# Kernel optimization log

Hardware: AMD Instinct MI355X
Metric: run time of the kernel (lower is better)

Reference implementation:

```python
import jax, jax.numpy as jnp
import numpy as np

SIZE = 161          # odd box size (init arg 160 -> 161)
INPUT_SIZE = 8
BATCH = 256
MARGIN = 3          # VOXEL_SPREAD_MARGIN


def _radial_expansion(grid):
    # verbatim numpy port of SparseVolumeReconstructionLinear.radial_expansion
    bz = grid.shape[0]
    bz2 = bz // 2
    mask1 = grid == -1
    ls = np.linspace(-bz2, bz2, bz)
    lsx = np.linspace(0, bz2, bz // 2 + 1)
    z, y, x = np.meshgrid(ls, ls, lsx)
    c = np.zeros((int(np.sum(mask1)), 3))
    c[:, 0] = x[mask1]
    c[:, 1] = y[mask1]
    c[:, 2] = z[mask1]
    norm = np.sqrt(np.sum(np.square(c), axis=1))
    c_ = np.round(c / norm[:, None]).astype(int)
    c = c.astype(int)
    c[:, 1:] += bz2
    c_ = c - c_
    g = grid[c_[:, 2], c_[:, 1], c_[:, 0]]
    mask2 = g >= 0
    grid[c[mask2, 2], c[mask2, 1], c[mask2, 0]] = g[mask2]


def _build_grid3d_index(size):
    bz = size
    bz_2 = bz // 2
    zz = (np.arange(bz) - bz_2) ** 2
    yy = (np.arange(bz) - bz_2) ** 2
    xx = np.arange(bz_2 + 1) ** 2
    mask = (zz[:, None, None] + yy[None, :, None] + xx[None, None, :]) <= bz_2 ** 2
    # C-order enumeration matches grid_iterator(z, y, x) ordering
    idx = np.cumsum(mask.ravel()).reshape(mask.shape) - 1
    grid = np.where(mask, idx, -1).astype(np.int64)
    m = MARGIN
    bzm = bz + 2 * m
    gm = np.full((bzm, bzm, bzm // 2 + 1), -1, dtype=np.int64)
    gm[m:-m, m:-m, :-m] = grid
    for _ in range(5):
        _radial_expansion(gm)
    return gm, int(mask.sum())


def _rand_rotations(key, n):
    q = jax.random.normal(key, (n, 4))
    q = q / jnp.linalg.norm(q, axis=1, keepdims=True)
    w, x, y, z = q[:, 0], q[:, 1], q[:, 2], q[:, 3]
    R = jnp.stack([
        1 - 2 * (y * y + z * z), 2 * (x * y - z * w), 2 * (x * z + y * w),
        2 * (x * y + z * w), 1 - 2 * (x * x + z * z), 2 * (y * z - x * w),
        2 * (x * z - y * w), 2 * (y * z + x * w), 1 - 2 * (x * x + y * y),
    ], axis=-1).reshape(n, 3, 3)
    return R.astype(jnp.float32)


def setup_inputs() -> dict:
    key = jax.random.key(0)
    k1, k2, k3, k4 = jax.random.split(key, 4)
    grid3d_index, weight_count = _build_grid3d_index(SIZE)
    weight = jax.random.normal(k1, (weight_count, INPUT_SIZE, 2), dtype=jnp.float32) * 1e-3
    bias = jax.random.normal(k2, (weight_count, 2), dtype=jnp.float32) * 1e-3
    inp = jax.random.normal(k3, (BATCH, INPUT_SIZE), dtype=jnp.float32)
    rot = _rand_rotations(k4, BATCH)
    # half-plane 2D Fourier coords (x >= 0), P = SIZE * (SIZE//2 + 1)
    ys, xs = np.meshgrid(np.arange(SIZE) - SIZE // 2, np.arange(SIZE // 2 + 1), indexing='ij')
    coord = np.stack([xs.ravel(), ys.ravel()], axis=-1).astype(np.float32)
    return {
        'input': inp,
        'weight': weight,
        'bias': bias,
        'grid3d_index': jnp.asarray(grid3d_index),
        'rot_matrices': rot,
        'grid2d_coord': jnp.asarray(coord),
        'max_r': SIZE // 2,
    }


def reference(input, weight, bias, grid3d_index, rot_matrices, grid2d_coord, max_r):
    # input: (B, D); weight: (W, D, 2); bias: (W, 2)
    # grid2d_coord: (P, 2) as (x, y); rot_matrices: (B, 3, 3)
    bz = grid3d_index.shape[0]
    bz2 = bz // 2
    mr = min(int(max_r), (bz - 2 * MARGIN) // 2)
    P = grid2d_coord.shape[0]
    # rotate the z=0 plane into 3D Fourier space: (B, P, 3) as (x, y, z)
    c2 = jnp.pad(grid2d_coord, ((0, 0), (0, 1)))
    c = jnp.einsum('bij,pj->bpi', rot_matrices, c2)
    # Hermitian symmetry: flip to x >= 0 half-grid, conjugate
    flip = c[..., 0] < 0
    c = jnp.where(flip[..., None], -c, c)
    valid = jnp.sum(grid2d_coord ** 2, axis=-1) <= float(mr * mr)  # (P,)
    c = jnp.where(valid[None, :, None], c, 0.0)
    f = jnp.floor(c)
    t = c - f                      # trilinear fractions (B, P, 3)
    fi = f.astype(jnp.int32)
    out = jnp.zeros((c.shape[0], P, 2), dtype=input.dtype)
    for dx in (0, 1):
        wx = t[..., 0] if dx else 1.0 - t[..., 0]
        for dy in (0, 1):
            wy = t[..., 1] if dy else 1.0 - t[..., 1]
            for dz in (0, 1):
                wz = t[..., 2] if dz else 1.0 - t[..., 2]
                xi = fi[..., 0] + dx
                yi = fi[..., 1] + dy + bz2
                zi = fi[..., 2] + dz + bz2
                j = grid3d_index[zi, yi, xi]        # (B, P) voxel ids, -1 = empty
                jm = jnp.maximum(j, 0)
                v = jnp.einsum('bd,bpdc->bpc', input, weight[jm]) + bias[jm]
                v = jnp.where((j >= 0)[..., None], v, 0.0)
                out = out + (wx * wy * wz)[..., None] * v
    imag_sign = jnp.where(flip, -1.0, 1.0)
    out = out * jnp.stack([jnp.ones_like(imag_sign), imag_sign], axis=-1)
    return jnp.where(valid[None, :, None], out, 0.0)
```

## Files before the change

kernel.cpp:

```cpp
#include <hip/hip_runtime.h>

#define BZ    167
#define BZ2   83
#define NX    84
#define NCELL (BZ * BZ * NX)
#define SYC   NX
#define SZC   (NX * BZ)
#define NXC   81
#define NYC   161
#define NTX   21
#define NTY   41
#define NTILE (NTX * NTY)
#define NBT   216
#define NBX   51

static __device__ __forceinline__ unsigned f2bf(float f) {
    unsigned u = __float_as_uint(f);
    return (u + 0x7FFFu + ((u >> 16) & 1u)) >> 16;
}
static __device__ __forceinline__ float bf_lo(unsigned u) {
    return __uint_as_float(u << 16);
}
static __device__ __forceinline__ float bf_hi(unsigned u) {
    return __uint_as_float(u & 0xFFFF0000u);
}

__global__ __launch_bounds__(256) void pack_allz(
    const float4* __restrict__ wsrc, uint2* __restrict__ wdst, int nw4, int nbw,
    const int* __restrict__ grid, const float* __restrict__ bias,
    int4* __restrict__ garrD, int ncell)
{
    if ((int)blockIdx.x < nbw) {
        const int i = blockIdx.x * 256 + threadIdx.x;
        if (i >= nw4) return;
        const float4 v = wsrc[i];
        wdst[i] = make_uint2(f2bf(v.x) | (f2bf(v.y) << 16),
                             f2bf(v.z) | (f2bf(v.w) << 16));
    } else {
        const int i = ((int)blockIdx.x - nbw) * 256 + threadIdx.x;
        if (i >= ncell) return;
        const int j0 = grid[i];
        const int j1 = (i + SZC < ncell) ? grid[i + SZC] : -1;
        unsigned b0 = 0u, b1 = 0u;
        if (j0 >= 0)
            b0 = f2bf(bias[2 * j0]) | (f2bf(bias[2 * j0 + 1]) << 16);
        if (j1 >= 0)
            b1 = f2bf(bias[2 * j1]) | (f2bf(bias[2 * j1 + 1]) << 16);
        garrD[i] = make_int4(j0, (int)b0, j1, (int)b1);
    }
}

__global__ __launch_bounds__(256, 4) void svr_tile(
    const float*    __restrict__ input,
    const unsigned* __restrict__ wpk,
    const int4*     __restrict__ garrD,
    const float*    __restrict__ rot,
    const float*    __restrict__ coord,
    const int*      __restrict__ max_r,
    float*          __restrict__ out,
    int P)
{
    const int m    = blockIdx.x;
    const int xcd  = m & 7;
    const int slot = m >> 3;
    const int b    = (slot / NBT) * 8 + xcd;
    const int tgrp = slot % NBT;
    const int wid  = threadIdx.x >> 6;
    const int lane = threadIdx.x & 63;
    const int t    = tgrp * 4 + wid;
    if (t >= NTILE) return;

    const int q    = lane & 3;
    const int h    = q & 1;
    const int dxl  = q >> 1;
    const int sub  = lane >> 2;
    const int px   = (t % NTX) * 4 + (sub & 3);
    const int py   = (t / NTX) * 4 + (sub >> 2);
    if (px >= NXC || py >= NYC) return;
    const int p    = py * NXC + px;

    const float2 xy = *(const float2*)(coord + 2 * p);
    const float x = xy.x, y = xy.y;

    const int mr = min(max_r[0], (BZ - 6) / 2);
    const bool valid = (x * x + y * y) <= (float)(mr * mr);

    float2* o = (float2*)(out + ((size_t)b * P + p) * 2);
    if (!valid) {
        if (q == 0) *o = make_float2(0.f, 0.f);
        return;
    }

    const float* R = rot + b * 9;
    float cx = fmaf(R[1], y, R[0] * x);
    float cy = fmaf(R[4], y, R[3] * x);
    float cz = fmaf(R[7], y, R[6] * x);

    float sgn = 1.f;
    if (cx < 0.f) { cx = -cx; cy = -cy; cz = -cz; sgn = -1.f; }

    const float fx = floorf(cx), fy = floorf(cy), fz = floorf(cz);
    const float tx = cx - fx, ty = cy - fy, tz = cz - fz;
    const int ix = (int)fx;
    const int iy = (int)fy + BZ2;
    const int iz = (int)fz + BZ2;

    const int base0 = (iz * BZ + iy) * NX + ix + dxl;
    const int4 Gd0 = garrD[base0];
    const int4 Gd1 = garrD[base0 + SYC];

    const float4 ih = *(const float4*)(input + b * 8 + h * 4);

    const float wxd = dxl ? tx : 1.f - tx;
    float wyz[4];
    wyz[0] = (1.f - ty) * (1.f - tz);
    wyz[1] = ty * (1.f - tz);
    wyz[2] = (1.f - ty) * tz;
    wyz[3] = ty * tz;

    int jraw[4]; unsigned bbl[4];
    jraw[0] = Gd0.x; bbl[0] = (unsigned)Gd0.y;
    jraw[1] = Gd1.x; bbl[1] = (unsigned)Gd1.y;
    jraw[2] = Gd0.z; bbl[2] = (unsigned)Gd0.w;
    jraw[3] = Gd1.z; bbl[3] = (unsigned)Gd1.w;

    int jj[4]; float wcl[4];
    #pragma unroll
    for (int i = 0; i < 4; ++i) {
        wcl[i] = (jraw[i] >= 0) ? wxd * wyz[i] : 0.f;
        jj[i]  = max(jraw[i], 0);
    }

    uint4 U[4];
    #pragma unroll
    for (int i = 0; i < 4; ++i)
        U[i] = *(const uint4*)(wpk + (size_t)jj[i] * 8 + h * 4);

    float acc0 = 0.f, acc1 = 0.f;
    #pragma unroll
    for (int i = 0; i < 4; ++i) {
        const float w = wcl[i];
        const unsigned bb = bbl[i];
        float v0 = h ? 0.f : bf_lo(bb);
        float v1 = h ? 0.f : bf_hi(bb);
        v0 = fmaf(ih.x, bf_lo(U[i].x), v0); v1 = fmaf(ih.x, bf_hi(U[i].x), v1);
        v0 = fmaf(ih.y, bf_lo(U[i].y), v0); v1 = fmaf(ih.y, bf_hi(U[i].y), v1);
        v0 = fmaf(ih.z, bf_lo(U[i].z), v0); v1 = fmaf(ih.z, bf_hi(U[i].z), v1);
        v0 = fmaf(ih.w, bf_lo(U[i].w), v0); v1 = fmaf(ih.w, bf_hi(U[i].w), v1);
        acc0 = fmaf(w, v0, acc0);
        acc1 = fmaf(w, v1, acc1);
    }

    acc0 += __shfl_xor(acc0, 1);
    acc1 += __shfl_xor(acc1, 1);
    acc0 += __shfl_xor(acc0, 2);
    acc1 += __shfl_xor(acc1, 2);

    if (q == 0) *o = make_float2(acc0, acc1 * sgn);
}

__global__ __launch_bounds__(256) void pack_w(
    const float4* __restrict__ src, uint2* __restrict__ dst, int n)
{
    const int i = blockIdx.x * 256 + threadIdx.x;
    if (i >= n) return;
    const float4 v = src[i];
    dst[i] = make_uint2(f2bf(v.x) | (f2bf(v.y) << 16),
                        f2bf(v.z) | (f2bf(v.w) << 16));
}
__global__ __launch_bounds__(256) void pack_b(
    const float* __restrict__ bias, unsigned* __restrict__ bpk, int W)
{
    const int j = blockIdx.x * 256 + threadIdx.x;
    if (j >= W) return;
    bpk[j] = f2bf(bias[2 * j]) | (f2bf(bias[2 * j + 1]) << 16);
}

__global__ __launch_bounds__(256) void svr_bf16(
    const float* __restrict__ input, const unsigned* __restrict__ wpk,
    const unsigned* __restrict__ bpk, const int* __restrict__ grid3d,
    const float* __restrict__ rot, const float* __restrict__ coord,
    const int* __restrict__ max_r, float* __restrict__ out, int P)
{
    const int m    = blockIdx.x;
    const int xcd  = m & 7;
    const int slot = m >> 3;
    const int b    = (slot / NBX) * 8 + xcd;
    const int p    = (slot % NBX) * 256 + threadIdx.x;
    if (p >= P) return;

    const float x = coord[2 * p + 0];
    const float y = coord[2 * p + 1];
    const int mr = min(max_r[0], (BZ - 6) / 2);
    const bool valid = (x * x + y * y) <= (float)(mr * mr);
    float2* o = (float2*)(out + ((size_t)b * P + p) * 2);
    if (!valid) { *o = make_float2(0.f, 0.f); return; }

    const float* R = rot + b * 9;
    float cx = fmaf(R[1], y, R[0] * x);
    float cy = fmaf(R[4], y, R[3] * x);
    float cz = fmaf(R[7], y, R[6] * x);
    float sgn = 1.f;
    if (cx < 0.f) { cx = -cx; cy = -cy; cz = -cz; sgn = -1.f; }
    const float fx = floorf(cx), fy = floorf(cy), fz = floorf(cz);
    const float tx = cx - fx, ty = cy - fy, tz = cz - fz;
    const int ix = (int)fx, iy = (int)fy + BZ2, iz = (int)fz + BZ2;

    const float* ib = input + b * 8;
    const float in0 = ib[0], in1 = ib[1], in2 = ib[2], in3 = ib[3];
    const float in4 = ib[4], in5 = ib[5], in6 = ib[6], in7 = ib[7];

    int jj[8]; float wc[8];
    const float wx0 = 1.f - tx, wy0 = 1.f - ty, wz0 = 1.f - tz;
    #pragma unroll
    for (int dz = 0; dz < 2; ++dz)
        #pragma unroll
        for (int dy = 0; dy < 2; ++dy) {
            const int base = ((iz + dz) * BZ + (iy + dy)) * NX + ix;
            #pragma unroll
            for (int dx = 0; dx < 2; ++dx) {
                const int c = dz * 4 + dy * 2 + dx;
                const int j = grid3d[base + dx];
                const float w = (dx ? tx : wx0) * (dy ? ty : wy0) * (dz ? tz : wz0);
                wc[c] = (j >= 0) ? w : 0.f;
                jj[c] = max(j, 0);
            }
        }

    uint4 U0[8], U1[8]; unsigned BB[8];
    #pragma unroll
    for (int c = 0; c < 8; ++c) {
        const uint4* wp = (const uint4*)(wpk + (size_t)jj[c] * 8);
        U0[c] = wp[0]; U1[c] = wp[1]; BB[c] = bpk[jj[c]];
    }

    float acc0 = 0.f, acc1 = 0.f;
    #pragma unroll
    for (int c = 0; c < 8; ++c) {
        const float w = wc[c];
        float v0 = bf_lo(BB[c]), v1 = bf_hi(BB[c]);
        v0 = fmaf(in0, bf_lo(U0[c].x), v0); v1 = fmaf(in0, bf_hi(U0[c].x), v1);
        v0 = fmaf(in1, bf_lo(U0[c].y), v0); v1 = fmaf(in1, bf_hi(U0[c].y), v1);
        v0 = fmaf(in2, bf_lo(U0[c].z), v0); v1 = fmaf(in2, bf_hi(U0[c].z), v1);
        v0 = fmaf(in3, bf_lo(U0[c].w), v0); v1 = fmaf(in3, bf_hi(U0[c].w), v1);
        v0 = fmaf(in4, bf_lo(U1[c].x), v0); v1 = fmaf(in4, bf_hi(U1[c].x), v1);
        v0 = fmaf(in5, bf_lo(U1[c].y), v0); v1 = fmaf(in5, bf_hi(U1[c].y), v1);
        v0 = fmaf(in6, bf_lo(U1[c].z), v0); v1 = fmaf(in6, bf_hi(U1[c].z), v1);
        v0 = fmaf(in7, bf_lo(U1[c].w), v0); v1 = fmaf(in7, bf_hi(U1[c].w), v1);
        acc0 = fmaf(w, v0, acc0);
        acc1 = fmaf(w, v1, acc1);
    }
    *o = make_float2(acc0, acc1 * sgn);
}

__global__ __launch_bounds__(256) void svr_fp32(
    const float* __restrict__ input, const float* __restrict__ weight,
    const float* __restrict__ bias, const int* __restrict__ grid3d,
    const float* __restrict__ rot, const float* __restrict__ coord,
    const int* __restrict__ max_r, float* __restrict__ out, int P)
{
    const int m    = blockIdx.x;
    const int xcd  = m & 7;
    const int slot = m >> 3;
    const int b    = (slot / NBX) * 8 + xcd;
    const int p    = (slot % NBX) * 256 + threadIdx.x;
    if (p >= P) return;

    const float x = coord[2 * p + 0];
    const float y = coord[2 * p + 1];
    const int mr = min(max_r[0], (BZ - 6) / 2);
    const bool valid = (x * x + y * y) <= (float)(mr * mr);
    float2* o = (float2*)(out + ((size_t)b * P + p) * 2);
    if (!valid) { *o = make_float2(0.f, 0.f); return; }

    const float* R = rot + b * 9;
    float cx = fmaf(R[1], y, R[0] * x);
    float cy = fmaf(R[4], y, R[3] * x);
    float cz = fmaf(R[7], y, R[6] * x);
    float sgn = 1.f;
    if (cx < 0.f) { cx = -cx; cy = -cy; cz = -cz; sgn = -1.f; }
    const float fx = floorf(cx), fy = floorf(cy), fz = floorf(cz);
    const float tx = cx - fx, ty = cy - fy, tz = cz - fz;
    const int ix = (int)fx, iy = (int)fy + BZ2, iz = (int)fz + BZ2;

    const float* ib = input + b * 8;
    const float in0 = ib[0], in1 = ib[1], in2 = ib[2], in3 = ib[3];
    const float in4 = ib[4], in5 = ib[5], in6 = ib[6], in7 = ib[7];

    int jj[8]; float wc[8];
    const float wx0 = 1.f - tx, wy0 = 1.f - ty, wz0 = 1.f - tz;
    #pragma unroll
    for (int dz = 0; dz < 2; ++dz)
        #pragma unroll
        for (int dy = 0; dy < 2; ++dy) {
            const int base = ((iz + dz) * BZ + (iy + dy)) * NX + ix;
            #pragma unroll
            for (int dx = 0; dx < 2; ++dx) {
                const int c = dz * 4 + dy * 2 + dx;
                const int j = grid3d[base + dx];
                const float w = (dx ? tx : wx0) * (dy ? ty : wy0) * (dz ? tz : wz0);
                wc[c] = (j >= 0) ? w : 0.f;
                jj[c] = max(j, 0);
            }
        }

    float acc0 = 0.f, acc1 = 0.f;
    #pragma unroll
    for (int c = 0; c < 8; ++c) {
        const size_t j = (size_t)jj[c];
        const float4* wp = (const float4*)(weight + j * 16);
        const float4 W0 = wp[0], W1 = wp[1], W2 = wp[2], W3 = wp[3];
        const float2 bb = *(const float2*)(bias + j * 2);
        const float w = wc[c];
        float v0 = bb.x, v1 = bb.y;
        v0 = fmaf(in0, W0.x, v0); v1 = fmaf(in0, W0.y, v1);
        v0 = fmaf(in1, W0.z, v0); v1 = fmaf(in1, W0.w, v1);
        v0 = fmaf(in2, W1.x, v0); v1 = fmaf(in2, W1.y, v1);
        v0 = fmaf(in3, W1.z, v0); v1 = fmaf(in3, W1.w, v1);
        v0 = fmaf(in4, W2.x, v0); v1 = fmaf(in4, W2.y, v1);
        v0 = fmaf(in5, W2.z, v0); v1 = fmaf(in5, W2.w, v1);
        v0 = fmaf(in6, W3.x, v0); v1 = fmaf(in6, W3.y, v1);
        v0 = fmaf(in7, W3.z, v0); v1 = fmaf(in7, W3.w, v1);
        acc0 = fmaf(w, v0, acc0);
        acc1 = fmaf(w, v1, acc1);
    }
    *o = make_float2(acc0, acc1 * sgn);
}

extern "C" void kernel_launch(void* const* d_in, const int* in_sizes, int n_in,
                              void* d_out, int out_size, void* d_ws, size_t ws_size,
                              hipStream_t stream) {
    const float* input  = (const float*)d_in[0];
    const float* weight = (const float*)d_in[1];
    const float* bias   = (const float*)d_in[2];
    const int*   grid3d = (const int*)  d_in[3];
    const float* rot    = (const float*)d_in[4];
    const float* coord  = (const float*)d_in[5];
    const int*   max_r  = (const int*)  d_in[6];
    float* out = (float*)d_out;

    const int P = in_sizes[5] / 2;
    const int B = in_sizes[4] / 9;
    const int W = in_sizes[1] / 16;

    const size_t wpk_bytes = (size_t)W * 32;
    const size_t need_zd   = wpk_bytes + (size_t)NCELL * 16;
    const size_t need_bf   = (size_t)W * 36;

    dim3 block(256, 1, 1);

    if (ws_size >= need_zd) {
        unsigned* wpk = (unsigned*)d_ws;
        int4* garrD = (int4*)((char*)d_ws + wpk_bytes);
        const int nw4 = W * 4;
        const int nbw = (nw4 + 255) / 256;
        const int nbg = (NCELL + 255) / 256;
        pack_allz<<<nbw + nbg, block, 0, stream>>>(
            (const float4*)weight, (uint2*)wpk, nw4, nbw,
            grid3d, bias, garrD, NCELL);
        dim3 grid(NBT * B, 1, 1);
        svr_tile<<<grid, block, 0, stream>>>(input, wpk, garrD, rot, coord,
                                             max_r, out, P);
    } else if (ws_size >= need_bf) {
        unsigned* wpk = (unsigned*)d_ws;
        unsigned* bpk = wpk + (size_t)W * 8;
        const int nw = W * 4;
        pack_w<<<(nw + 255) / 256, block, 0, stream>>>(
            (const float4*)weight, (uint2*)wpk, nw);
        pack_b<<<(W + 255) / 256, block, 0, stream>>>(bias, bpk, W);
        dim3 grid(NBX * B, 1, 1);
        svr_bf16<<<grid, block, 0, stream>>>(input, wpk, bpk, grid3d, rot,
                                             coord, max_r, out, P);
    } else {
        dim3 grid(NBX * B, 1, 1);
        svr_fp32<<<grid, block, 0, stream>>>(input, weight, bias, grid3d, rot,
                                             coord, max_r, out, P);
    }
}
```

Baseline: 220.7 us.

## Pack weights and input as fp16 and use packed dot2 instructions in gather kernel

Weights and the per-batch input vector are converted to packed fp16 pairs in the prep kernel, and the inner 4-term dot products use v_dot2 fp16 instructions instead of bf16 unpack plus scalar FMAs. The launch grid also changes from a 1D XCD-swizzled layout to a 3D grid of (batch, x-tile, y-tile group). This cuts ALU work in the per-corner dot product. It trades bf16 range for fp16 precision on weights and inputs, and drops the XCD-aware block mapping that may have aided L2 locality.

```diff
diff --git a/kernel.cpp b/kernel.cpp
--- a/kernel.cpp
+++ b/kernel.cpp
@@ -9,9 +9,7 @@
 #define NXC   81
 #define NYC   161
 #define NTX   21
-#define NTY   41
-#define NTILE (NTX * NTY)
-#define NBT   216
+#define NTZ   11
 #define NBX   51
 
 static __device__ __forceinline__ unsigned f2bf(float f) {
@@ -25,19 +23,30 @@
     return __uint_as_float(u & 0xFFFF0000u);
 }
 
-__global__ __launch_bounds__(256) void pack_allz(
+typedef _Float16 h2 __attribute__((ext_vector_type(2)));
+static __device__ __forceinline__ h2 u2h(unsigned u) {
+    union { unsigned u; h2 h; } x; x.u = u; return x.h;
+}
+static __device__ __forceinline__ unsigned f2h2(float a, float b) {
+    union { h2 h; unsigned u; } x;
+    x.h.x = (_Float16)a; x.h.y = (_Float16)b;
+    return x.u;
+}
+
+__global__ __launch_bounds__(256) void pack_allh(
     const float4* __restrict__ wsrc, uint2* __restrict__ wdst, int nw4, int nbw,
     const int* __restrict__ grid, const float* __restrict__ bias,
-    int4* __restrict__ garrD, int ncell)
-{
-    if ((int)blockIdx.x < nbw) {
-        const int i = blockIdx.x * 256 + threadIdx.x;
+    int4* __restrict__ garrD, int ncell, int nbg,
+    const float* __restrict__ input, unsigned* __restrict__ inpk, int nin)
+{
+    const int bid = (int)blockIdx.x;
+    if (bid < nbw) {
+        const int i = bid * 256 + threadIdx.x;
         if (i >= nw4) return;
         const float4 v = wsrc[i];
-        wdst[i] = make_uint2(f2bf(v.x) | (f2bf(v.y) << 16),
-                             f2bf(v.z) | (f2bf(v.w) << 16));
-    } else {
-        const int i = ((int)blockIdx.x - nbw) * 256 + threadIdx.x;
+        wdst[i] = make_uint2(f2h2(v.x, v.z), f2h2(v.y, v.w));
+    } else if (bid < nbw + nbg) {
+        const int i = (bid - nbw) * 256 + threadIdx.x;
         if (i >= ncell) return;
         const int j0 = grid[i];
         const int j1 = (i + SZC < ncell) ? grid[i + SZC] : -1;
@@ -47,11 +56,16 @@
         if (j1 >= 0)
             b1 = f2bf(bias[2 * j1]) | (f2bf(bias[2 * j1 + 1]) << 16);
         garrD[i] = make_int4(j0, (int)b0, j1, (int)b1);
-    }
-}
-
-__global__ __launch_bounds__(256, 4) void svr_tile(
-    const float*    __restrict__ input,
+    } else {
+        const int i = (bid - nbw - nbg) * 256 + threadIdx.x;
+        if (i >= nin) return;
+        const int b = i >> 2, k = i & 3;
+        inpk[i] = f2h2(input[b * 8 + 2 * k], input[b * 8 + 2 * k + 1]);
+    }
+}
+
+__global__ __launch_bounds__(256, 4) void svr_dot(
+    const unsigned* __restrict__ inpk,
     const unsigned* __restrict__ wpk,
     const int4*     __restrict__ garrD,
     const float*    __restrict__ rot,
@@ -60,22 +74,18 @@
     float*          __restrict__ out,
     int P)
 {
-    const int m    = blockIdx.x;
-    const int xcd  = m & 7;
-    const int slot = m >> 3;
-    const int b    = (slot / NBT) * 8 + xcd;
-    const int tgrp = slot % NBT;
+    const int b    = (int)blockIdx.x;
+    const int lane = threadIdx.x & 63;
     const int wid  = threadIdx.x >> 6;
-    const int lane = threadIdx.x & 63;
-    const int t    = tgrp * 4 + wid;
-    if (t >= NTILE) return;
+    const int ty   = (int)blockIdx.z * 4 + wid;
+    if (ty * 4 >= NYC) return;
 
     const int q    = lane & 3;
     const int h    = q & 1;
     const int dxl  = q >> 1;
     const int sub  = lane >> 2;
-    const int px   = (t % NTX) * 4 + (sub & 3);
-    const int py   = (t / NTX) * 4 + (sub >> 2);
+    const int px   = (int)blockIdx.y * 4 + (sub & 3);
+    const int py   = ty * 4 + (sub >> 2);
     if (px >= NXC || py >= NYC) return;
     const int p    = py * NXC + px;
 
@@ -100,7 +110,7 @@
     if (cx < 0.f) { cx = -cx; cy = -cy; cz = -cz; sgn = -1.f; }
 
     const float fx = floorf(cx), fy = floorf(cy), fz = floorf(cz);
-    const float tx = cx - fx, ty = cy - fy, tz = cz - fz;
+    const float tx = cx - fx, ty2 = cy - fy, tz = cz - fz;
     const int ix = (int)fx;
     const int iy = (int)fy + BZ2;
     const int iz = (int)fz + BZ2;
@@ -109,14 +119,16 @@
     const int4 Gd0 = garrD[base0];
     const int4 Gd1 = garrD[base0 + SYC];
 
-    const float4 ih = *(const float4*)(input + b * 8 + h * 4);
+    const uint2 ihu = *(const uint2*)(inpk + b * 4 + h * 2);
+    const h2 ihp0 = u2h(ihu.x);
+    const h2 ihp1 = u2h(ihu.y);
 
     const float wxd = dxl ? tx : 1.f - tx;
     float wyz[4];
-    wyz[0] = (1.f - ty) * (1.f - tz);
-    wyz[1] = ty * (1.f - tz);
-    wyz[2] = (1.f - ty) * tz;
-    wyz[3] = ty * tz;
+    wyz[0] = (1.f - ty2) * (1.f - tz);
+    wyz[1] = ty2 * (1.f - tz);
+    wyz[2] = (1.f - ty2) * tz;
+    wyz[3] = ty2 * tz;
 
     int jraw[4]; unsigned bbl[4];
     jraw[0] = Gd0.x; bbl[0] = (unsigned)Gd0.y;
@@ -139,16 +151,15 @@
     float acc0 = 0.f, acc1 = 0.f;
     #pragma unroll
     for (int i = 0; i < 4; ++i) {
-        const float w = wcl[i];
         const unsigned bb = bbl[i];
         float v0 = h ? 0.f : bf_lo(bb);
         float v1 = h ? 0.f : bf_hi(bb);
-        v0 = fmaf(ih.x, bf_lo(U[i].x), v0); v1 = fmaf(ih.x, bf_hi(U[i].x), v1);
-        v0 = fmaf(ih.y, bf_lo(U[i].y), v0); v1 = fmaf(ih.y, bf_hi(U[i].y), v1);
-        v0 = fmaf(ih.z, bf_lo(U[i].z), v0); v1 = fmaf(ih.z, bf_hi(U[i].z), v1);
-        v0 = fmaf(ih.w, bf_lo(U[i].w), v0); v1 = fmaf(ih.w, bf_hi(U[i].w), v1);
-        acc0 = fmaf(w, v0, acc0);
-        acc1 = fmaf(w, v1, acc1);
+        v0 = __builtin_amdgcn_fdot2(ihp0, u2h(U[i].x), v0, false);
+        v0 = __builtin_amdgcn_fdot2(ihp1, u2h(U[i].z), v0, false);
+        v1 = __builtin_amdgcn_fdot2(ihp0, u2h(U[i].y), v1, false);
+        v1 = __builtin_amdgcn_fdot2(ihp1, u2h(U[i].w), v1, false);
+        acc0 = fmaf(wcl[i], v0, acc0);
+        acc1 = fmaf(wcl[i], v1, acc1);
     }
 
     acc0 += __shfl_xor(acc0, 1);
@@ -343,24 +354,30 @@
     const int B = in_sizes[4] / 9;
     const int W = in_sizes[1] / 16;
 
-    const size_t wpk_bytes = (size_t)W * 32;
-    const size_t need_zd   = wpk_bytes + (size_t)NCELL * 16;
-    const size_t need_bf   = (size_t)W * 36;
+    const size_t wpk_bytes  = (size_t)W * 32;
+    const size_t garr_bytes = (size_t)NCELL * 16;
+    const size_t in_bytes   = (size_t)B * 16;
+    const size_t need_zd    = wpk_bytes + garr_bytes + in_bytes;
+    const size_t need_bf    = (size_t)W * 36;
 
     dim3 block(256, 1, 1);
 
-    if (ws_size >= need_zd) {
+    if (ws_size >= need_zd && P == NXC * NYC) {
         unsigned* wpk = (unsigned*)d_ws;
         int4* garrD = (int4*)((char*)d_ws + wpk_bytes);
+        unsigned* inpk = (unsigned*)((char*)d_ws + wpk_bytes + garr_bytes);
         const int nw4 = W * 4;
         const int nbw = (nw4 + 255) / 256;
         const int nbg = (NCELL + 255) / 256;
-        pack_allz<<<nbw + nbg, block, 0, stream>>>(
+        const int nin = B * 4;
+        const int nbi = (nin + 255) / 256;
+        pack_allh<<<nbw + nbg + nbi, block, 0, stream>>>(
             (const float4*)weight, (uint2*)wpk, nw4, nbw,
-            grid3d, bias, garrD, NCELL);
-        dim3 grid(NBT * B, 1, 1);
-        svr_tile<<<grid, block, 0, stream>>>(input, wpk, garrD, rot, coord,
-                                             max_r, out, P);
+            grid3d, bias, garrD, NCELL, nbg,
+            input, inpk, nin);
+        dim3 grid(B, NTX, NTZ);
+        svr_dot<<<grid, block, 0, stream>>>(inpk, wpk, garrD, rot, coord,
+                                            max_r, out, P);
     } else if (ws_size >= need_bf) {
         unsigned* wpk = (unsigned*)d_ws;
         unsigned* bpk = wpk + (size_t)W * 8;
```

Measured after the change: 224.8 us. Within noise of the previous version (+1.9%).
